# Optimization experiments

Hardware: AMD Instinct MI355X
Metric: run time of the kernel (lower is better)

Reference implementation:

```python
import jax, jax.numpy as jnp
import numpy as np

D_MODEL = 256
N_HEADS = 8
D_HEAD = D_MODEL // N_HEADS
B = 65536
LN_EPS = 1e-5


def setup_inputs() -> dict:
    key = jax.random.key(0)
    ks = jax.random.split(key, 6)
    s = 1.0 / np.sqrt(D_MODEL)
    x = jax.random.normal(ks[0], (B, D_MODEL), dtype=jnp.float32)
    Wq = jax.random.normal(ks[1], (D_MODEL, D_MODEL), dtype=jnp.float32) * s
    Wk = jax.random.normal(ks[2], (D_MODEL, D_MODEL), dtype=jnp.float32) * s
    Wv = jax.random.normal(ks[3], (D_MODEL, D_MODEL), dtype=jnp.float32) * s
    Wout = jax.random.normal(ks[4], (D_MODEL, D_MODEL), dtype=jnp.float32) * s
    b_out = jnp.zeros((D_MODEL,), dtype=jnp.float32)
    # L initialized to identity per head (matches nn.init.eye_) plus tiny noise
    L = jnp.broadcast_to(jnp.eye(D_HEAD, dtype=jnp.float32), (N_HEADS, D_HEAD, D_HEAD)) \
        + 0.01 * jax.random.normal(ks[5], (N_HEADS, D_HEAD, D_HEAD), dtype=jnp.float32)
    gamma = jnp.ones((D_MODEL,), dtype=jnp.float32)
    beta = jnp.zeros((D_MODEL,), dtype=jnp.float32)
    return {"x": x, "Wq": Wq, "Wk": Wk, "Wv": Wv, "Wout": Wout,
            "b_out": b_out, "L": L, "gamma": gamma, "beta": beta}


def reference(x, Wq, Wk, Wv, Wout, b_out, L, gamma, beta):
    b = x.shape[0]
    # projections; view as [B, H, d_head]
    Q = (x @ Wq).reshape(b, N_HEADS, D_HEAD)
    K = (x @ Wk).reshape(b, N_HEADS, D_HEAD)
    V = (x @ Wv).reshape(b, N_HEADS, D_HEAD)
    # pairwise head differences: [B, Hq, Hk, d_head]
    diff = Q[:, :, None, :] - K[:, None, :, :]
    # per-key-head learned metric transform: L indexed by key head
    diff_t = jnp.einsum('bqkd,kdf->bqkf', diff, L)
    sq_dist = jnp.sum(diff_t * diff_t, axis=-1)            # [B, Hq, Hk]
    attn = jax.nn.softmax(-sq_dist / jnp.sqrt(jnp.float32(D_HEAD)), axis=2)
    out = jnp.einsum('bqk,bkd->bqd', attn, V).reshape(b, D_MODEL)
    out = out @ Wout + b_out
    h = out + x
    # LayerNorm over last dim
    mu = jnp.mean(h, axis=-1, keepdims=True)
    var = jnp.mean((h - mu) ** 2, axis=-1, keepdims=True)
    return (h - mu) * jax.lax.rsqrt(var + LN_EPS) * gamma + beta
```

## Files before the change

### kernel.cpp

```cpp
#include <hip/hip_runtime.h>


typedef __bf16 bf16x8 __attribute__((ext_vector_type(8)));
typedef __bf16 bf16x2 __attribute__((ext_vector_type(2)));
typedef float  f32x4  __attribute__((ext_vector_type(4)));
typedef int    i32x4  __attribute__((ext_vector_type(4)));
typedef int    i32x2  __attribute__((ext_vector_type(2)));
typedef unsigned short u16;

__device__ __forceinline__ u16 f2bf(float f){
  __bf16 b = (__bf16)f;
  return __builtin_bit_cast(u16, b);
}
__device__ __forceinline__ unsigned int pk2(float lo, float hi){
  bf16x2 v; v[0] = (__bf16)lo; v[1] = (__bf16)hi;
  return __builtin_bit_cast(unsigned int, v);
}
__device__ __forceinline__ bf16x8 ldfrag_lds(const u16* p){
  return __builtin_bit_cast(bf16x8, *(const i32x4*)p);
}
__device__ __forceinline__ bf16x8 ldfrag_g(const u16* p){
  return __builtin_bit_cast(bf16x8, *(const i32x4*)p);
}

#define LROW 264

__device__ __forceinline__ int kts_off(int k, int r, int fb){
  return (k*2048 + r*64 + fb*2) ^ ((r & 7) << 4);
}

__global__ __launch_bounds__(256) void geo_prep(
    const float* __restrict__ Wq, const float* __restrict__ Wk,
    const float* __restrict__ Wv, const float* __restrict__ Wout,
    const float* __restrict__ L, u16* __restrict__ ws)
{
  const int b = blockIdx.x, t = threadIdx.x;
  if (b < 64){
    const int m = b >> 4;
    const float* src = (m == 0) ? Wq : (m == 1) ? Wk : (m == 2) ? Wv : Wout;
    u16* dstbase = (m < 3) ? (ws + m*65536) : (ws + 196608);
    const int tile = b & 15;
    const int tr = tile >> 2, tc = tile & 3;
    __shared__ float tlf[64][68];
    {
      const int row = t >> 2, cs = (t & 3)*16;
      #pragma unroll
      for (int j = 0; j < 4; ++j){
        f32x4 v = *(const f32x4*)(src + (size_t)(tr*64 + row)*256 + tc*64 + cs + j*4);
        #pragma unroll
        for (int p = 0; p < 4; ++p) tlf[row][cs + j*4 + p] = v[p];
      }
    }
    __syncthreads();
    {
      const int n = t >> 2, cs = (t & 3)*16;
      float us[16];
      if (m == 1){
        const int hh = n >> 5, f = n & 31;
        const int kg = tc*2 + hh;
        #pragma unroll
        for (int j = 0; j < 16; ++j) us[j] = 0.f;
        #pragma unroll 4
        for (int d = 0; d < 32; ++d){
          const float lv = L[kg*1024 + d*32 + f];
          #pragma unroll
          for (int j = 0; j < 16; ++j)
            us[j] = fmaf(tlf[cs + j][hh*32 + d], lv, us[j]);
        }
      } else {
        #pragma unroll
        for (int j = 0; j < 16; ++j) us[j] = tlf[cs + j][n];
      }
      #pragma unroll
      for (int h = 0; h < 2; ++h){
        i32x4 o;
        #pragma unroll
        for (int p = 0; p < 4; ++p)
          o[p] = (int)pk2(us[h*8 + 2*p], us[h*8 + 2*p + 1]);
        *(i32x4*)(dstbase + (size_t)(tc*64 + n)*256 + tr*64 + cs + h*8) = o;
      }
    }
  } else {
    u16* Lt = ws + 262144;
    const int k = t >> 5, f = t & 31;
    for (int d = 0; d < 32; ++d)
      Lt[k*1024 + f*32 + d] = f2bf(L[k*1024 + d*32 + f]);
  }
}

__global__ __launch_bounds__(512, 6) void geo_fused(
    const float* __restrict__ x,     const u16* __restrict__ WqkvT,
    const u16* __restrict__ WoutT,   const u16* __restrict__ Lt,
    const float* __restrict__ b_out, const float* __restrict__ gamma,
    const float* __restrict__ beta,  float* __restrict__ out)
{
  __shared__ __align__(16) char pool[50688];
  u16*  xsU  = (u16*)(pool);
  char* ktsB = pool;
  u16*  hsU  = (u16*)(pool);
  u16*  QsU  = (u16*)(pool + 16896);
  u16*  aoU  = (u16*)(pool + 16896);
  u16*  VsU  = (u16*)(pool + 33792);

  const int t    = threadIdx.x;
  const int lane = t & 63;
  const int w    = t >> 6;
  const int l15  = lane & 15;
  const int quad = lane >> 4;
  const long rowbase = (long)blockIdx.x * 32;

  {
    const int r  = t >> 4;
    const int c0 = (t & 15) * 16;
    const float* src = x + (rowbase + r)*256 + c0;
    unsigned int wds[8];
    #pragma unroll
    for (int j = 0; j < 4; ++j){
      f32x4 v = *(const f32x4*)(src + j*4);
      wds[j*2    ] = pk2(v[0], v[1]);
      wds[j*2 + 1] = pk2(v[2], v[3]);
    }
    #pragma unroll
    for (int h = 0; h < 2; ++h){
      i32x4 o;
      #pragma unroll
      for (int p = 0; p < 4; ++p) o[p] = (int)wds[h*4 + p];
      *(i32x4*)&xsU[r*LROW + c0 + h*8] = o;
    }
  }
  __syncthreads();

  #pragma unroll
  for (int si = 0; si < 2; ++si){
    const int s = si << 1;
    const u16* Bbase = WqkvT + (size_t)(s*256 + w*32)*256;
    u16* dst = si ? VsU : QsU;
    f32x4 acc[2][2];
    #pragma unroll
    for (int mt = 0; mt < 2; ++mt)
      #pragma unroll
      for (int nt = 0; nt < 2; ++nt) acc[mt][nt] = f32x4{0.f,0.f,0.f,0.f};
    #pragma unroll
    for (int kk = 0; kk < 8; ++kk){
      const int c0 = kk*32 + quad*8;
      bf16x8 a[2], bb[2];
      #pragma unroll
      for (int mt = 0; mt < 2; ++mt) a[mt] = ldfrag_lds(&xsU[(mt*16 + l15)*LROW + c0]);
      #pragma unroll
      for (int nt = 0; nt < 2; ++nt) bb[nt] = ldfrag_g(Bbase + (size_t)(nt*16 + l15)*256 + c0);
      #pragma unroll
      for (int mt = 0; mt < 2; ++mt)
        #pragma unroll
        for (int nt = 0; nt < 2; ++nt)
          acc[mt][nt] = __builtin_amdgcn_mfma_f32_16x16x32_bf16(a[mt], bb[nt], acc[mt][nt], 0, 0, 0);
    }
    #pragma unroll
    for (int mt = 0; mt < 2; ++mt)
      #pragma unroll
      for (int nt = 0; nt < 2; ++nt){
        const int col = w*32 + nt*16 + l15;
        #pragma unroll
        for (int reg = 0; reg < 4; ++reg)
          dst[(mt*16 + quad*4 + reg)*LROW + col] = f2bf(acc[mt][nt][reg]);
      }
  }

  f32x4 kacc[2][2];
  {
    #pragma unroll
    for (int mt = 0; mt < 2; ++mt)
      #pragma unroll
      for (int nt = 0; nt < 2; ++nt) kacc[mt][nt] = f32x4{0.f,0.f,0.f,0.f};
    const u16* Abase = WqkvT + (size_t)(256 + w*32)*256;
    #pragma unroll
    for (int kk = 0; kk < 8; ++kk){
      const int c0 = kk*32 + quad*8;
      bf16x8 aW[2], bX[2];
      #pragma unroll
      for (int mt = 0; mt < 2; ++mt) aW[mt] = ldfrag_g(Abase + (size_t)(mt*16 + l15)*256 + c0);
      #pragma unroll
      for (int nt = 0; nt < 2; ++nt) bX[nt] = ldfrag_lds(&xsU[(nt*16 + l15)*LROW + c0]);
      #pragma unroll
      for (int mt = 0; mt < 2; ++mt)
        #pragma unroll
        for (int nt = 0; nt < 2; ++nt)
          kacc[mt][nt] = __builtin_amdgcn_mfma_f32_16x16x32_bf16(aW[mt], bX[nt], kacc[mt][nt], 0, 0, 0);
    }
  }
  __syncthreads();

  {
    #pragma unroll
    for (int mt = 0; mt < 2; ++mt)
      #pragma unroll
      for (int nt = 0; nt < 2; ++nt){
        const int r = nt*16 + l15;
        i32x2 o;
        o[0] = (int)pk2(kacc[mt][nt][0], kacc[mt][nt][1]);
        o[1] = (int)pk2(kacc[mt][nt][2], kacc[mt][nt][3]);
        *(i32x2*)(ktsB + kts_off(w, r, mt*16 + quad*4)) = o;
      }
  }
  __syncthreads();

  float lg[2][8];
  {
    bf16x8 bQ[2];
    #pragma unroll
    for (int nt = 0; nt < 2; ++nt)
      bQ[nt] = ldfrag_lds(&QsU[(nt*16 + l15)*LROW + w*32 + quad*8]);
    #pragma unroll
    for (int k = 0; k < 8; ++k){
      bf16x8 aL[2];
      #pragma unroll
      for (int mt = 0; mt < 2; ++mt)
        aL[mt] = ldfrag_g(Lt + k*1024 + (mt*16 + l15)*32 + quad*8);
      f32x4 acc[2][2];
      #pragma unroll
      for (int mt = 0; mt < 2; ++mt)
        #pragma unroll
        for (int nt = 0; nt < 2; ++nt)
          acc[mt][nt] = __builtin_amdgcn_mfma_f32_16x16x32_bf16(aL[mt], bQ[nt],
                          f32x4{0.f,0.f,0.f,0.f}, 0, 0, 0);
      #pragma unroll
      for (int nt = 0; nt < 2; ++nt){
        const int r = nt*16 + l15;
        float s = 0.f;
        #pragma unroll
        for (int mt = 0; mt < 2; ++mt){
          i32x2 kt2 = *(const i32x2*)(ktsB + kts_off(k, r, mt*16 + quad*4));
          unsigned int u0 = (unsigned int)kt2[0], u1 = (unsigned int)kt2[1];
          float kv0 = __builtin_bit_cast(float, u0 << 16);
          float kv1 = __builtin_bit_cast(float, u0 & 0xFFFF0000u);
          float kv2 = __builtin_bit_cast(float, u1 << 16);
          float kv3 = __builtin_bit_cast(float, u1 & 0xFFFF0000u);
          float d0 = acc[mt][nt][0] - kv0, d1 = acc[mt][nt][1] - kv1;
          float d2 = acc[mt][nt][2] - kv2, d3 = acc[mt][nt][3] - kv3;
          s = fmaf(d0, d0, s); s = fmaf(d1, d1, s);
          s = fmaf(d2, d2, s); s = fmaf(d3, d3, s);
        }
        s += __shfl_xor(s, 16);
        s += __shfl_xor(s, 32);
        lg[nt][k] = s * -0.17677669529663687f;
      }
    }
  }

  {
    #pragma unroll
    for (int nt = 0; nt < 2; ++nt){
      const int r = nt*16 + l15;
      float mx = lg[nt][0];
      #pragma unroll
      for (int k = 1; k < 8; ++k) mx = fmaxf(mx, lg[nt][k]);
      float e[8], sum = 0.f;
      #pragma unroll
      for (int k = 0; k < 8; ++k){ e[k] = __expf(lg[nt][k] - mx); sum += e[k]; }
      const float inv = 1.0f / sum;
      float o[8] = {0.f,0.f,0.f,0.f,0.f,0.f,0.f,0.f};
      #pragma unroll
      for (int k = 0; k < 8; ++k){
        i32x4 v = *(const i32x4*)&VsU[r*LROW + k*32 + quad*8];
        const float a = e[k] * inv;
        #pragma unroll
        for (int p = 0; p < 4; ++p){
          unsigned int u = (unsigned int)v[p];
          o[2*p    ] = fmaf(a, __builtin_bit_cast(float, u << 16),         o[2*p    ]);
          o[2*p + 1] = fmaf(a, __builtin_bit_cast(float, u & 0xFFFF0000u), o[2*p + 1]);
        }
      }
      i32x4 pkv;
      #pragma unroll
      for (int p = 0; p < 4; ++p) pkv[p] = (int)pk2(o[2*p], o[2*p + 1]);
      *(i32x4*)&aoU[r*LROW + w*32 + quad*8] = pkv;
    }
  }

  f32x4 xpre[4];
  #pragma unroll
  for (int rr = 0; rr < 4; ++rr)
    xpre[rr] = *(const f32x4*)(x + (rowbase + w*4 + rr)*256 + lane*4);

  __syncthreads();

  {
    f32x4 acc[2][2];
    #pragma unroll
    for (int mt = 0; mt < 2; ++mt)
      #pragma unroll
      for (int nt = 0; nt < 2; ++nt) acc[mt][nt] = f32x4{0.f,0.f,0.f,0.f};
    #pragma unroll
    for (int kk = 0; kk < 8; ++kk){
      const int c0 = kk*32 + quad*8;
      bf16x8 a[2], bb[2];
      #pragma unroll
      for (int mt = 0; mt < 2; ++mt) a[mt] = ldfrag_lds(&aoU[(mt*16 + l15)*LROW + c0]);
      #pragma unroll
      for (int nt = 0; nt < 2; ++nt)
        bb[nt] = ldfrag_g(WoutT + (size_t)(w*32 + nt*16 + l15)*256 + c0);
      #pragma unroll
      for (int mt = 0; mt < 2; ++mt)
        #pragma unroll
        for (int nt = 0; nt < 2; ++nt)
          acc[mt][nt] = __builtin_amdgcn_mfma_f32_16x16x32_bf16(a[mt], bb[nt], acc[mt][nt], 0, 0, 0);
    }
    #pragma unroll
    for (int nt = 0; nt < 2; ++nt){
      const int col = w*32 + nt*16 + l15;
      const float bo = b_out[col];
      #pragma unroll
      for (int mt = 0; mt < 2; ++mt)
        #pragma unroll
        for (int reg = 0; reg < 4; ++reg)
          hsU[(mt*16 + quad*4 + reg)*LROW + col] = f2bf(acc[mt][nt][reg] + bo);
    }
  }
  __syncthreads();

  {
    #pragma unroll
    for (int rr = 0; rr < 4; ++rr){
      const int r = w*4 + rr;
      const int c = lane*4;
      i32x2 h2 = *(const i32x2*)&hsU[r*LROW + c];
      f32x4 xv = xpre[rr];
      unsigned int u0 = (unsigned int)h2[0], u1 = (unsigned int)h2[1];
      f32x4 hv;
      hv[0] = __builtin_bit_cast(float, u0 << 16)         + xv[0];
      hv[1] = __builtin_bit_cast(float, u0 & 0xFFFF0000u) + xv[1];
      hv[2] = __builtin_bit_cast(float, u1 << 16)         + xv[2];
      hv[3] = __builtin_bit_cast(float, u1 & 0xFFFF0000u) + xv[3];
      float s  = hv[0] + hv[1] + hv[2] + hv[3];
      float s2 = hv[0]*hv[0] + hv[1]*hv[1] + hv[2]*hv[2] + hv[3]*hv[3];
      #pragma unroll
      for (int off = 1; off < 64; off <<= 1){
        s  += __shfl_xor(s,  off);
        s2 += __shfl_xor(s2, off);
      }
      const float mu  = s  * (1.0f/256.0f);
      const float var = s2 * (1.0f/256.0f) - mu*mu;
      const float rs  = rsqrtf(var + 1e-5f);
      f32x4 gv = *(const f32x4*)(gamma + c);
      f32x4 bv = *(const f32x4*)(beta  + c);
      f32x4 y;
      y[0] = (hv[0] - mu)*rs*gv[0] + bv[0];
      y[1] = (hv[1] - mu)*rs*gv[1] + bv[1];
      y[2] = (hv[2] - mu)*rs*gv[2] + bv[2];
      y[3] = (hv[3] - mu)*rs*gv[3] + bv[3];
      *(f32x4*)(out + (rowbase + r)*256 + c) = y;
    }
  }
}

extern "C" void kernel_launch(void* const* d_in, const int* in_sizes, int n_in,
                              void* d_out, int out_size, void* d_ws, size_t ws_size,
                              hipStream_t stream)
{
  const float* x     = (const float*)d_in[0];
  const float* Wq    = (const float*)d_in[1];
  const float* Wk    = (const float*)d_in[2];
  const float* Wv    = (const float*)d_in[3];
  const float* Wout  = (const float*)d_in[4];
  const float* b_out = (const float*)d_in[5];
  const float* L     = (const float*)d_in[6];
  const float* gamma = (const float*)d_in[7];
  const float* beta  = (const float*)d_in[8];
  u16* ws = (u16*)d_ws;

  geo_prep<<<65, 256, 0, stream>>>(Wq, Wk, Wv, Wout, L, ws);
  geo_fused<<<2048, 512, 0, stream>>>(x, ws, ws + 196608, ws + 262144,
                                      b_out, gamma, beta, (float*)d_out);
}
```

Before: 261.0 us.

## Keep Q fragments in registers via shuffles and shrink shared memory pool

Q is now computed transposed, with the weights as the A operand and x as B. Its accumulator is repacked into the B-operand fragment layout with cross-lane shuffles, so the Q tile no longer goes through shared memory. This lets the LDS pool drop from about 50KB to 33KB and the launch bound rise to 8 blocks per CU, aiming for higher occupancy and fewer LDS round trips. In exchange it adds shuffle work, a new barrier before aliased buffers are reused, and tighter register limits that may cause spills.

```diff
diff --git a/kernel.cpp b/kernel.cpp
--- a/kernel.cpp
+++ b/kernel.cpp
@@ -88,19 +88,18 @@
   }
 }
 
-__global__ __launch_bounds__(512, 6) void geo_fused(
+__global__ __launch_bounds__(512, 8) void geo_fused(
     const float* __restrict__ x,     const u16* __restrict__ WqkvT,
     const u16* __restrict__ WoutT,   const u16* __restrict__ Lt,
     const float* __restrict__ b_out, const float* __restrict__ gamma,
     const float* __restrict__ beta,  float* __restrict__ out)
 {
-  __shared__ __align__(16) char pool[50688];
+  __shared__ __align__(16) char pool[33792];
   u16*  xsU  = (u16*)(pool);
   char* ktsB = pool;
-  u16*  hsU  = (u16*)(pool);
-  u16*  QsU  = (u16*)(pool + 16896);
-  u16*  aoU  = (u16*)(pool + 16896);
-  u16*  VsU  = (u16*)(pool + 33792);
+  u16*  aoU  = (u16*)(pool);
+  u16*  VsU  = (u16*)(pool + 16896);
+  u16*  hsU  = (u16*)(pool + 16896);
 
   const int t    = threadIdx.x;
   const int lane = t & 63;
@@ -130,11 +129,48 @@
   }
   __syncthreads();
 
-  #pragma unroll
-  for (int si = 0; si < 2; ++si){
-    const int s = si << 1;
-    const u16* Bbase = WqkvT + (size_t)(s*256 + w*32)*256;
-    u16* dst = si ? VsU : QsU;
+  bf16x8 bQ[2];
+  {
+    f32x4 qacc[2][2];
+    #pragma unroll
+    for (int mt = 0; mt < 2; ++mt)
+      #pragma unroll
+      for (int nt = 0; nt < 2; ++nt) qacc[mt][nt] = f32x4{0.f,0.f,0.f,0.f};
+    const u16* Abase = WqkvT + (size_t)(w*32)*256;
+    #pragma unroll
+    for (int kk = 0; kk < 8; ++kk){
+      const int c0 = kk*32 + quad*8;
+      bf16x8 aW[2], bX[2];
+      #pragma unroll
+      for (int mt = 0; mt < 2; ++mt) aW[mt] = ldfrag_g(Abase + (size_t)(mt*16 + l15)*256 + c0);
+      #pragma unroll
+      for (int nt = 0; nt < 2; ++nt) bX[nt] = ldfrag_lds(&xsU[(nt*16 + l15)*LROW + c0]);
+      #pragma unroll
+      for (int mt = 0; mt < 2; ++mt)
+        #pragma unroll
+        for (int nt = 0; nt < 2; ++nt)
+          qacc[mt][nt] = __builtin_amdgcn_mfma_f32_16x16x32_bf16(aW[mt], bX[nt], qacc[mt][nt], 0, 0, 0);
+    }
+    #pragma unroll
+    for (int nt = 0; nt < 2; ++nt){
+      const unsigned int s00 = pk2(qacc[0][nt][0], qacc[0][nt][1]);
+      const unsigned int s01 = pk2(qacc[0][nt][2], qacc[0][nt][3]);
+      const unsigned int s10 = pk2(qacc[1][nt][0], qacc[1][nt][1]);
+      const unsigned int s11 = pk2(qacc[1][nt][2], qacc[1][nt][3]);
+      i32x4 bq;
+      #pragma unroll
+      for (int j2 = 0; j2 < 4; ++j2){
+        const int srcl = (((quad & 1)*2 + (j2 >> 1)) << 4) + l15;
+        const int v0 = __shfl((int)((j2 & 1) ? s01 : s00), srcl, 64);
+        const int v1 = __shfl((int)((j2 & 1) ? s11 : s10), srcl, 64);
+        bq[j2] = (quad < 2) ? v0 : v1;
+      }
+      bQ[nt] = __builtin_bit_cast(bf16x8, bq);
+    }
+  }
+
+  {
+    const u16* Bbase = WqkvT + (size_t)(512 + w*32)*256;
     f32x4 acc[2][2];
     #pragma unroll
     for (int mt = 0; mt < 2; ++mt)
@@ -161,7 +197,7 @@
         const int col = w*32 + nt*16 + l15;
         #pragma unroll
         for (int reg = 0; reg < 4; ++reg)
-          dst[(mt*16 + quad*4 + reg)*LROW + col] = f2bf(acc[mt][nt][reg]);
+          VsU[(mt*16 + quad*4 + reg)*LROW + col] = f2bf(acc[mt][nt][reg]);
       }
   }
 
@@ -205,10 +241,6 @@
 
   float lg[2][8];
   {
-    bf16x8 bQ[2];
-    #pragma unroll
-    for (int nt = 0; nt < 2; ++nt)
-      bQ[nt] = ldfrag_lds(&QsU[(nt*16 + l15)*LROW + w*32 + quad*8]);
     #pragma unroll
     for (int k = 0; k < 8; ++k){
       bf16x8 aL[2];
@@ -245,6 +277,7 @@
       }
     }
   }
+  __syncthreads();
 
   {
     #pragma unroll
```

Result: slower. 330.3 us (+26.5%).
